# Performance work log

Measured on AMD Instinct MI355X. Metric: run time of the kernel, lower is better.

## Reference

```python
import jax, jax.numpy as jnp
import numpy as np

N = 200000
SIZE = 16384
IN = 128
OUT = 128
HEADS = 4
SLOPE = 0.01  # nn.LeakyReLU default


def setup_inputs() -> dict:
    key = jax.random.key(0)
    ks = jax.random.split(key, 12)
    s = 0.05
    inp = {
        "fea": jax.random.normal(ks[0], (N, IN), jnp.float32),
        "cry_fea": jax.random.normal(ks[1], (SIZE, IN), jnp.float32),
        # MH_M: per-head MLP in->in->out (grouped conv1d k=1, groups=heads)
        "W_m1": jax.random.normal(ks[2], (HEADS, IN, IN), jnp.float32) * s,
        "b_m1": jax.random.normal(ks[3], (HEADS, IN), jnp.float32) * s,
        "W_m2": jax.random.normal(ks[4], (HEADS, OUT, IN), jnp.float32) * s,
        "b_m2": jax.random.normal(ks[5], (HEADS, OUT), jnp.float32) * s,
        # MH_A: per-head MLP 2*in->in->1 (scalar attention, vector_attention=False)
        "W_a1": jax.random.normal(ks[6], (HEADS, IN, 2 * IN), jnp.float32) * s,
        "b_a1": jax.random.normal(ks[7], (HEADS, IN), jnp.float32) * s,
        "W_a2": jax.random.normal(ks[8], (HEADS, 1, IN), jnp.float32) * s,
        "b_a2": jax.random.normal(ks[9], (HEADS, 1), jnp.float32) * s,
        "index": jnp.sort(jax.random.randint(ks[10], (N,), 0, SIZE, jnp.int32)),
        "size": SIZE,
    }
    return inp


def _leaky(x):
    return jnp.where(x >= 0, x, SLOPE * x)


def _mh_mlp(x, W1, b1, W2, b2):
    # x: [N, d_in]; per-head linear -> leaky -> linear. Returns [N, H, d_out].
    h = _leaky(jnp.einsum("ni,hoi->nho", x, W1) + b1)
    return jnp.einsum("nhi,hoi->nho", h, W2) + b2


def reference(fea, cry_fea, W_m1, b_m1, W_m2, b_m2, W_a1, b_a1, W_a2, b_a2, index, size):
    # message transform m: [N, H, OUT]
    m = _mh_mlp(fea, W_m1, b_m1, W_m2, b_m2)
    # attention input: concat(node fea, gathered crystal fea) -> [N, 2*IN]
    a_in = jnp.concatenate([fea, cry_fea[index]], axis=-1)
    alpha = _mh_mlp(a_in, W_a1, b_a1, W_a2, b_a2)  # [N, H, 1]
    # segment (per-crystal) softmax over nodes sharing the same index
    amax = jax.ops.segment_max(alpha, index, num_segments=size)
    amax = jnp.where(jnp.isfinite(amax), amax, 0.0)
    e = jnp.exp(alpha - amax[index])
    denom = jax.ops.segment_sum(e, index, num_segments=size)
    alpha = e / (denom[index] + 1e-16)
    # weighted scatter-add aggregation -> [size, H*OUT]
    out = jax.ops.segment_sum((alpha * m).reshape(-1, HEADS * OUT), index, num_segments=size)
    return out
```

## Files before the change

### kernel.cpp

```cpp
#include <hip/hip_runtime.h>

typedef __bf16 bf16x8 __attribute__((ext_vector_type(8)));
typedef float  f32x4  __attribute__((ext_vector_type(4)));
typedef unsigned int u32x4 __attribute__((ext_vector_type(4)));

#define MFMA(a, b, c) __builtin_amdgcn_mfma_f32_16x16x32_bf16((a), (b), (c), 0, 0, 0)

#define THREADS 512
#define WAVES   8
#define CPW     4
#define CPB     32
#define MT      32

#define SEG_INTS  16416
#define SEG_BYTES (SEG_INTS * 4)
#define O_WM1 0
#define O_WM2 65536
#define O_WA1 131072
#define O_WA2 262144
#define W_ELEMS 262656
#define W_BYTES (W_ELEMS * 2)

#define LA1B 0
#define LM1B 65536
#define LM2B 98304

__device__ __forceinline__ bf16x8 cvt8(const float* pf) {
    float4 a = *(const float4*)pf, b = *(const float4*)(pf + 4);
    bf16x8 o;
    o[0] = (__bf16)a.x; o[1] = (__bf16)a.y; o[2] = (__bf16)a.z; o[3] = (__bf16)a.w;
    o[4] = (__bf16)b.x; o[5] = (__bf16)b.y; o[6] = (__bf16)b.z; o[7] = (__bf16)b.w;
    return o;
}

__device__ __forceinline__ unsigned pk2(float a, float b) {
    unsigned short ua = __builtin_bit_cast(unsigned short, (__bf16)a);
    unsigned short ub = __builtin_bit_cast(unsigned short, (__bf16)b);
    return (unsigned)ua | ((unsigned)ub << 16);
}

__device__ __forceinline__ int lower_bound(const int* __restrict__ a, int n, int v) {
    int lo = 0, hi = n;
    while (lo < hi) { int mid = (lo + hi) >> 1; if (a[mid] < v) lo = mid + 1; else hi = mid; }
    return lo;
}

__global__ __launch_bounds__(256) void prep_kernel(
    const float* __restrict__ Wm1, const float* __restrict__ Wm2,
    const float* __restrict__ Wa1, const float* __restrict__ Wa2,
    __bf16* __restrict__ wb)
{
    int i8 = blockIdx.x * 256 + threadIdx.x;
    if (i8 >= W_ELEMS / 8) return;
    int i = i8 * 8;
    const float* src; int s;
    if      (i < O_WM2) { src = Wm1; s = i; }
    else if (i < O_WA1) { src = Wm2; s = i - O_WM2; }
    else if (i < O_WA2) { src = Wa1; s = i - O_WA1; }
    else                { src = Wa2; s = i - O_WA2; }
    *(bf16x8*)(wb + i) = cvt8(src + s);
}

__global__ __launch_bounds__(256) void seg_kernel(
    const int* __restrict__ index, int N, int S, int* __restrict__ seg)
{
    int c = blockIdx.x * 256 + threadIdx.x;
    if (c <= S) seg[c] = lower_bound(index, N, c);
}

__global__ __launch_bounds__(256) void cast_kernel(
    const float* __restrict__ src, __bf16* __restrict__ dst, int n8)
{
    int i = blockIdx.x * 256 + threadIdx.x;
    if (i < n8) *(bf16x8*)(dst + (size_t)i * 8) = cvt8(src + (size_t)i * 8);
}

template<bool WB, bool SEG, bool FB>
__global__ __launch_bounds__(THREADS, 2) void fused4_kernel(
    const float* __restrict__ fea, const float* __restrict__ cry,
    const float* __restrict__ Wm1, const float* __restrict__ bm1,
    const float* __restrict__ Wm2, const float* __restrict__ bm2,
    const float* __restrict__ Wa1, const float* __restrict__ ba1,
    const float* __restrict__ Wa2, const float* __restrict__ ba2,
    const __bf16* __restrict__ wb, const int* __restrict__ seg,
    const __bf16* __restrict__ feab, const __bf16* __restrict__ cryb,
    const int* __restrict__ index, int N, int S, float* __restrict__ out)
{
    __shared__ __align__(16) __bf16 wlds[65536];
    __shared__ float crylds[WAVES][CPW][128];
    __shared__ float bm1lds[128];

    const int h  = blockIdx.x & 3;
    const int c0 = (blockIdx.x >> 2) * CPB;
    const int t  = threadIdx.x;
    const int lane = t & 63, w = t >> 6, ml = lane & 15, q = lane >> 4;
    const int swzb = (ml & 7) << 4;
    const char* wbytes = (const char*)wlds;

#pragma unroll
    for (int i = 0; i < 16; i++) {
        const int cb = (t + i * THREADS) << 4;
        int local, row, slot, rowE; size_t wboff; const float* basef;
        if (cb < LM1B)      { local = cb;        row = local >> 9; slot = (local >> 4) & 31; rowE = 256; wboff = (size_t)O_WA1 + (size_t)h * 32768; basef = Wa1 + (size_t)h * 32768; }
        else if (cb < LM2B) { local = cb - LM1B; row = local >> 8; slot = (local >> 4) & 15; rowE = 128; wboff = (size_t)O_WM1 + (size_t)h * 16384; basef = Wm1 + (size_t)h * 16384; }
        else                { local = cb - LM2B; row = local >> 8; slot = (local >> 4) & 15; rowE = 128; wboff = (size_t)O_WM2 + (size_t)h * 16384; basef = Wm2 + (size_t)h * 16384; }
        size_t off = (size_t)row * rowE + (size_t)((slot ^ (row & 7)) << 3);
        bf16x8 v;
        if constexpr (WB) v = *(const bf16x8*)(wb + wboff + off);
        else              v = cvt8(basef + off);
        *(bf16x8*)((char*)wlds + cb) = v;
    }
    if (t < 32) *(float4*)&bm1lds[t * 4] = *(const float4*)&bm1[h * 128 + t * 4];
    __syncthreads();

    const int cw0 = min(c0 + w * CPW, S);
    const int cw1 = min(cw0 + CPW, S);
    int start, end;
    if constexpr (SEG) { start = seg[cw0]; end = seg[cw1]; }
    else { start = lower_bound(index, N, cw0); end = lower_bound(index, N, cw1); }

    float ba1v[8], bb2[8], wa2v[8];
#pragma unroll
    for (int ot = 0; ot < 8; ot++) {
        ba1v[ot] = ba1[h * 128 + ot * 16 + ml];
        bb2[ot]  = bm2[h * 128 + ot * 16 + ml];
        wa2v[ot] = Wa2[h * 128 + ot * 16 + ml];
    }
    const float ba2v = ba2[h];

    {
        bf16x8 cf[4];
#pragma unroll
        for (int kk = 0; kk < 4; kk++) {
            bf16x8 z;
#pragma unroll
            for (int j = 0; j < 8; j++) z[j] = (__bf16)0.f;
            if (ml < CPW && cw0 + ml < S) {
                if constexpr (FB) z = *(const bf16x8*)(cryb + (size_t)(cw0 + ml) * 128 + kk * 32 + q * 8);
                else              z = cvt8(cry + (size_t)(cw0 + ml) * 128 + kk * 32 + q * 8);
            }
            cf[kk] = z;
        }
#pragma unroll
        for (int ot = 0; ot < 8; ot++) {
            f32x4 acc = {0.f, 0.f, 0.f, 0.f};
#pragma unroll
            for (int kk = 0; kk < 4; kk++) {
                bf16x8 B = *(const bf16x8*)(wbytes + LA1B + (ot * 16 + ml) * 512 + ((((16 + kk * 4 + q) << 4)) ^ swzb));
                acc = MFMA(cf[kk], B, acc);
            }
            if (q == 0) {
#pragma unroll
                for (int r = 0; r < 4; r++) crylds[w][r][ot * 16 + ml] = acc[r];
            }
        }
    }

    float m_run = -1e30f, d_run = 0.f;
    float wacc[8] = {0.f,0.f,0.f,0.f,0.f,0.f,0.f,0.f};
    int cur_c = -1, emit_c = cw0;

    auto flushf = [&]() {
        float inv = 1.f / (d_run + 1e-16f);
        for (int z = emit_c; z < cur_c; z++)
            *(float2*)&out[(size_t)z * 512 + h * 128 + lane * 2] = make_float2(0.f, 0.f);
#pragma unroll
        for (int ot = 0; ot < 8; ot++) {
            float v = wacc[ot];
            v += __shfl_xor(v, 16);
            v += __shfl_xor(v, 32);
            if (q == 0) out[(size_t)cur_c * 512 + h * 128 + ot * 16 + ml] = v * inv;
            wacc[ot] = 0.f;
        }
        emit_c = cur_c + 1;
        m_run = -1e30f; d_run = 0.f;
    };

    for (int tb = start; tb < end; tb += MT) {
        int nv = end - tb; if (nv > MT) nv = MT;

        const int iv = (lane < nv) ? index[tb + lane] : cw0;

        unsigned long long bmask;
        {
            int ivp = __shfl(iv, lane > 0 ? lane - 1 : 0);
            bmask = __ballot(lane < nv && (lane == 0 || iv != ivp));
        }

        for (int s = 0; s < 2; s++) {
            const int lo = s * 16;
            if (lo >= nv) break;
            int hcnt = nv - lo; if (hcnt > 16) hcnt = 16;

            bf16x8 afh[4];
            {
                const int row = lo + ml;
                const bool val = row < nv;
#pragma unroll
                for (int kk = 0; kk < 4; kk++) {
                    bf16x8 z;
#pragma unroll
                    for (int j = 0; j < 8; j++) z[j] = (__bf16)0.f;
                    if (val) {
                        if constexpr (FB) z = *(const bf16x8*)(feab + (size_t)(tb + row) * 128 + kk * 32 + q * 8);
                        else              z = cvt8(fea + (size_t)(tb + row) * 128 + kk * 32 + q * 8);
                    }
                    afh[kk] = z;
                }
            }

            float lv4[4];
            {
                int cl4[4];
#pragma unroll
                for (int r = 0; r < 4; r++)
                    cl4[r] = __shfl(iv, lo + q * 4 + r) - cw0;
                float lsum[4] = {0.f, 0.f, 0.f, 0.f};
#pragma unroll
                for (int ot = 0; ot < 8; ot++) {
                    bf16x8 B[4];
#pragma unroll
                    for (int kk = 0; kk < 4; kk++)
                        B[kk] = *(const bf16x8*)(wbytes + LA1B + (ot * 16 + ml) * 512 + ((((kk * 4 + q) << 4)) ^ swzb));
                    const int oc = ot * 16 + ml;
                    f32x4 acc;
#pragma unroll
                    for (int r = 0; r < 4; r++) acc[r] = crylds[w][cl4[r]][oc];
#pragma unroll
                    for (int kk = 0; kk < 4; kk++) acc = MFMA(afh[kk], B[kk], acc);
#pragma unroll
                    for (int r = 0; r < 4; r++) {
                        float v = acc[r] + ba1v[ot]; v = v >= 0.f ? v : 0.01f * v;
                        lsum[r] += v * wa2v[ot];
                    }
                }
#pragma unroll
                for (int rr = 0; rr < 4; rr++) {
                    float x = lsum[rr];
                    x += __shfl_xor(x, 1); x += __shfl_xor(x, 2);
                    x += __shfl_xor(x, 4); x += __shfl_xor(x, 8);
                    lv4[rr] = x + ba2v;
                }
            }

            bf16x8 a2h[4];
#pragma unroll
            for (int kk = 0; kk < 4; kk++) {
                unsigned pw[2][2];
#pragma unroll
                for (int otl = 0; otl < 2; otl++) {
                    const int ot = kk * 2 + otl;
                    bf16x8 A[4];
#pragma unroll
                    for (int k4 = 0; k4 < 4; k4++)
                        A[k4] = *(const bf16x8*)(wbytes + LM1B + (ot * 16 + ml) * 256 + ((((k4 * 4 + q) << 4)) ^ swzb));
                    const float4 bq = *(const float4*)&bm1lds[ot * 16 + q * 4];
                    f32x4 acc = {0.f, 0.f, 0.f, 0.f};
#pragma unroll
                    for (int k4 = 0; k4 < 4; k4++) acc = MFMA(A[k4], afh[k4], acc);
                    float v0 = acc[0] + bq.x, v1 = acc[1] + bq.y;
                    float v2 = acc[2] + bq.z, v3 = acc[3] + bq.w;
                    v0 = v0 >= 0.f ? v0 : 0.01f * v0;  v1 = v1 >= 0.f ? v1 : 0.01f * v1;
                    v2 = v2 >= 0.f ? v2 : 0.01f * v2;  v3 = v3 >= 0.f ? v3 : 0.01f * v3;
                    pw[otl][0] = pk2(v0, v1);
                    pw[otl][1] = pk2(v2, v3);
                }
                const int srcLo = (((2 * q) & 3) << 4) + ml;
                const int srcHi = (((2 * q + 1) & 3) << 4) + ml;
                const bool hiSel = (q >> 1) & 1;
                unsigned l0a = (unsigned)__shfl((int)pw[0][0], srcLo);
                unsigned l0b = (unsigned)__shfl((int)pw[1][0], srcLo);
                unsigned l1a = (unsigned)__shfl((int)pw[0][1], srcLo);
                unsigned l1b = (unsigned)__shfl((int)pw[1][1], srcLo);
                unsigned h0a = (unsigned)__shfl((int)pw[0][0], srcHi);
                unsigned h0b = (unsigned)__shfl((int)pw[1][0], srcHi);
                unsigned h1a = (unsigned)__shfl((int)pw[0][1], srcHi);
                unsigned h1b = (unsigned)__shfl((int)pw[1][1], srcHi);
                u32x4 wv4u = { hiSel ? l0b : l0a, hiSel ? l1b : l1a,
                               hiSel ? h0b : h0a, hiSel ? h1b : h1a };
                a2h[kk] = __builtin_bit_cast(bf16x8, wv4u);
            }

            f32x4 acc2h[8];
#pragma unroll
            for (int ot = 0; ot < 8; ot++) {
                bf16x8 B[4];
#pragma unroll
                for (int kk = 0; kk < 4; kk++)
                    B[kk] = *(const bf16x8*)(wbytes + LM2B + (ot * 16 + ml) * 256 + ((((kk * 4 + q) << 4)) ^ swzb));
                f32x4 acc = {bb2[ot], bb2[ot], bb2[ot], bb2[ot]};
#pragma unroll
                for (int kk = 0; kk < 4; kk++) acc = MFMA(a2h[kk], B[kk], acc);
                acc2h[ot] = acc;
            }

            unsigned hm = (unsigned)((bmask >> lo) & 0xffffull) | 1u;
            if (hcnt < 16) hm &= (1u << hcnt) - 1u;
            while (hm) {
                int a = (int)__builtin_ctz(hm);
                hm &= hm - 1u;
                int b = hm ? (int)__builtin_ctz(hm) : hcnt;
                int c = __shfl(iv, lo + a);
                if (c != cur_c) {
                    if (cur_c >= 0) flushf();
                    cur_c = c;
                }
                float tmax = -1e30f;
#pragma unroll
                for (int rr = 0; rr < 4; rr++) {
                    int row = q * 4 + rr;
                    if (row >= a && row < b) tmax = fmaxf(tmax, lv4[rr]);
                }
                tmax = fmaxf(tmax, __shfl_xor(tmax, 16));
                tmax = fmaxf(tmax, __shfl_xor(tmax, 32));
                float m_new = fmaxf(m_run, tmax);
                float scf = __expf(m_run - m_new);
                d_run *= scf;
#pragma unroll
                for (int ot = 0; ot < 8; ot++) wacc[ot] *= scf;
                m_run = m_new;

                float wv4[4]; float dp = 0.f;
#pragma unroll
                for (int rr = 0; rr < 4; rr++) {
                    int row = q * 4 + rr;
                    float ww = (row >= a && row < b) ? __expf(lv4[rr] - m_run) : 0.f;
                    wv4[rr] = ww; dp += ww;
                }
                dp += __shfl_xor(dp, 16);
                dp += __shfl_xor(dp, 32);
                d_run += dp;
#pragma unroll
                for (int ot = 0; ot < 8; ot++) {
                    f32x4 acc = acc2h[ot];
                    wacc[ot] += wv4[0] * acc[0] + wv4[1] * acc[1]
                              + wv4[2] * acc[2] + wv4[3] * acc[3];
                }
            }
        }
    }

    if (cur_c >= 0) flushf();
    for (int z = emit_c; z < cw1; z++)
        *(float2*)&out[(size_t)z * 512 + h * 128 + lane * 2] = make_float2(0.f, 0.f);
}

extern "C" void kernel_launch(void* const* d_in, const int* in_sizes, int n_in,
                              void* d_out, int out_size, void* d_ws, size_t ws_size,
                              hipStream_t stream)
{
    const float* fea = (const float*)d_in[0];
    const float* cry = (const float*)d_in[1];
    const float* Wm1 = (const float*)d_in[2];
    const float* bm1 = (const float*)d_in[3];
    const float* Wm2 = (const float*)d_in[4];
    const float* bm2 = (const float*)d_in[5];
    const float* Wa1 = (const float*)d_in[6];
    const float* ba1 = (const float*)d_in[7];
    const float* Wa2 = (const float*)d_in[8];
    const float* ba2 = (const float*)d_in[9];
    const int* index = (const int*)d_in[10];

    const int N = in_sizes[0] / 128;
    const int S = out_size / 512;
    const int grid = 4 * ((S + CPB - 1) / CPB);

    const size_t wOff    = (size_t)SEG_BYTES;
    const size_t cryOff  = wOff + (size_t)W_BYTES;
    const size_t feaOff  = cryOff + (size_t)S * 256;
    const size_t needSeg  = (size_t)SEG_BYTES;
    const size_t needW    = cryOff;
    const size_t needFull = feaOff + (size_t)N * 256;
    const bool segFits = (S + 1) <= SEG_INTS;

    if (segFits && ws_size >= needFull) {
        int* seg = (int*)d_ws;
        __bf16* wbp  = (__bf16*)((char*)d_ws + wOff);
        __bf16* cryb = (__bf16*)((char*)d_ws + cryOff);
        __bf16* feab = (__bf16*)((char*)d_ws + feaOff);
        seg_kernel<<<(S + 1 + 255) / 256, 256, 0, stream>>>(index, N, S, seg);
        prep_kernel<<<(W_ELEMS / 8 + 255) / 256, 256, 0, stream>>>(Wm1, Wm2, Wa1, Wa2, wbp);
        cast_kernel<<<(S * 16 + 255) / 256, 256, 0, stream>>>(cry, cryb, S * 16);
        cast_kernel<<<(N * 16 + 255) / 256, 256, 0, stream>>>(fea, feab, N * 16);
        fused4_kernel<true, true, true><<<grid, THREADS, 0, stream>>>(
            fea, cry, Wm1, bm1, Wm2, bm2, Wa1, ba1, Wa2, ba2,
            wbp, seg, feab, cryb, index, N, S, (float*)d_out);
    } else if (segFits && ws_size >= needW) {
        int* seg = (int*)d_ws;
        __bf16* wbp = (__bf16*)((char*)d_ws + wOff);
        seg_kernel<<<(S + 1 + 255) / 256, 256, 0, stream>>>(index, N, S, seg);
        prep_kernel<<<(W_ELEMS / 8 + 255) / 256, 256, 0, stream>>>(Wm1, Wm2, Wa1, Wa2, wbp);
        fused4_kernel<true, true, false><<<grid, THREADS, 0, stream>>>(
            fea, cry, Wm1, bm1, Wm2, bm2, Wa1, ba1, Wa2, ba2,
            wbp, seg, nullptr, nullptr, index, N, S, (float*)d_out);
    } else if (segFits && ws_size >= needSeg) {
        int* seg = (int*)d_ws;
        seg_kernel<<<(S + 1 + 255) / 256, 256, 0, stream>>>(index, N, S, seg);
        fused4_kernel<false, true, false><<<grid, THREADS, 0, stream>>>(
            fea, cry, Wm1, bm1, Wm2, bm2, Wa1, ba1, Wa2, ba2,
            nullptr, seg, nullptr, nullptr, index, N, S, (float*)d_out);
    } else {
        fused4_kernel<false, false, false><<<grid, THREADS, 0, stream>>>(
            fea, cry, Wm1, bm1, Wm2, bm2, Wa1, ba1, Wa2, ba2,
            nullptr, nullptr, nullptr, nullptr, index, N, S, (float*)d_out);
    }
}
```

Before: 411.3 us.

## Drop fp32-to-bf16 activation cast kernels, merge prep launches, shrink LDS weights

Removes the separate kernels that cast fea and cry_fea to bf16. The fused kernel now reads fp32 activations and converts them in-register, which avoids a full extra read and write pass over the 200k-row feature matrix. The seg and weight-pack kernels are merged into one launch. Only the node half of Wa1 is now kept in LDS (the crystal half is read from global memory), cutting shared memory to 96KB. That lets blocks grow to 1024 threads and 64 crystals each, with a higher occupancy hint. The cost is twice the global bytes for fea inside the main kernel and uncached global reads for the crystal-side weights.

```diff
diff --git a/kernel.cpp b/kernel.cpp
--- a/kernel.cpp
+++ b/kernel.cpp
@@ -6,10 +6,10 @@
 
 #define MFMA(a, b, c) __builtin_amdgcn_mfma_f32_16x16x32_bf16((a), (b), (c), 0, 0, 0)
 
-#define THREADS 512
-#define WAVES   8
+#define THREADS 1024
+#define WAVES   16
 #define CPW     4
-#define CPB     32
+#define CPB     64
 #define MT      32
 
 #define SEG_INTS  16416
@@ -22,8 +22,8 @@
 #define W_BYTES (W_ELEMS * 2)
 
 #define LA1B 0
-#define LM1B 65536
-#define LM2B 98304
+#define LM1B 32768
+#define LM2B 65536
 
 __device__ __forceinline__ bf16x8 cvt8(const float* pf) {
     float4 a = *(const float4*)pf, b = *(const float4*)(pf + 4);
@@ -45,48 +45,40 @@
     return lo;
 }
 
-__global__ __launch_bounds__(256) void prep_kernel(
+__global__ __launch_bounds__(256) void prep2_kernel(
     const float* __restrict__ Wm1, const float* __restrict__ Wm2,
     const float* __restrict__ Wa1, const float* __restrict__ Wa2,
-    __bf16* __restrict__ wb)
+    const int* __restrict__ index, int N, int S, int segBlocks,
+    int* __restrict__ seg, __bf16* __restrict__ wb, int doPack)
 {
-    int i8 = blockIdx.x * 256 + threadIdx.x;
-    if (i8 >= W_ELEMS / 8) return;
-    int i = i8 * 8;
-    const float* src; int s;
-    if      (i < O_WM2) { src = Wm1; s = i; }
-    else if (i < O_WA1) { src = Wm2; s = i - O_WM2; }
-    else if (i < O_WA2) { src = Wa1; s = i - O_WA1; }
-    else                { src = Wa2; s = i - O_WA2; }
-    *(bf16x8*)(wb + i) = cvt8(src + s);
-}
-
-__global__ __launch_bounds__(256) void seg_kernel(
-    const int* __restrict__ index, int N, int S, int* __restrict__ seg)
-{
-    int c = blockIdx.x * 256 + threadIdx.x;
-    if (c <= S) seg[c] = lower_bound(index, N, c);
-}
-
-__global__ __launch_bounds__(256) void cast_kernel(
-    const float* __restrict__ src, __bf16* __restrict__ dst, int n8)
-{
-    int i = blockIdx.x * 256 + threadIdx.x;
-    if (i < n8) *(bf16x8*)(dst + (size_t)i * 8) = cvt8(src + (size_t)i * 8);
-}
-
-template<bool WB, bool SEG, bool FB>
-__global__ __launch_bounds__(THREADS, 2) void fused4_kernel(
+    const int b = blockIdx.x;
+    if (b < segBlocks) {
+        int c = b * 256 + threadIdx.x;
+        if (c <= S) seg[c] = lower_bound(index, N, c);
+    } else if (doPack) {
+        int i8 = (b - segBlocks) * 256 + threadIdx.x;
+        if (i8 >= W_ELEMS / 8) return;
+        int i = i8 * 8;
+        const float* src; int s;
+        if      (i < O_WM2) { src = Wm1; s = i; }
+        else if (i < O_WA1) { src = Wm2; s = i - O_WM2; }
+        else if (i < O_WA2) { src = Wa1; s = i - O_WA1; }
+        else                { src = Wa2; s = i - O_WA2; }
+        *(bf16x8*)(wb + i) = cvt8(src + s);
+    }
+}
+
+template<bool WB, bool SEG>
+__global__ __launch_bounds__(THREADS, 4) void fused5_kernel(
     const float* __restrict__ fea, const float* __restrict__ cry,
     const float* __restrict__ Wm1, const float* __restrict__ bm1,
     const float* __restrict__ Wm2, const float* __restrict__ bm2,
     const float* __restrict__ Wa1, const float* __restrict__ ba1,
     const float* __restrict__ Wa2, const float* __restrict__ ba2,
     const __bf16* __restrict__ wb, const int* __restrict__ seg,
-    const __bf16* __restrict__ feab, const __bf16* __restrict__ cryb,
     const int* __restrict__ index, int N, int S, float* __restrict__ out)
 {
-    __shared__ __align__(16) __bf16 wlds[65536];
+    __shared__ __align__(16) __bf16 wlds[49152];
     __shared__ float crylds[WAVES][CPW][128];
     __shared__ float bm1lds[128];
 
@@ -98,16 +90,23 @@
     const char* wbytes = (const char*)wlds;
 
 #pragma unroll
-    for (int i = 0; i < 16; i++) {
+    for (int i = 0; i < 6; i++) {
         const int cb = (t + i * THREADS) << 4;
-        int local, row, slot, rowE; size_t wboff; const float* basef;
-        if (cb < LM1B)      { local = cb;        row = local >> 9; slot = (local >> 4) & 31; rowE = 256; wboff = (size_t)O_WA1 + (size_t)h * 32768; basef = Wa1 + (size_t)h * 32768; }
-        else if (cb < LM2B) { local = cb - LM1B; row = local >> 8; slot = (local >> 4) & 15; rowE = 128; wboff = (size_t)O_WM1 + (size_t)h * 16384; basef = Wm1 + (size_t)h * 16384; }
-        else                { local = cb - LM2B; row = local >> 8; slot = (local >> 4) & 15; rowE = 128; wboff = (size_t)O_WM2 + (size_t)h * 16384; basef = Wm2 + (size_t)h * 16384; }
-        size_t off = (size_t)row * rowE + (size_t)((slot ^ (row & 7)) << 3);
+        const int r = cb >> 15;
+        const int local = cb & 32767;
+        const int row = local >> 8;
+        const int col8 = ((((local >> 4) & 15) ^ (row & 7)) << 3);
         bf16x8 v;
-        if constexpr (WB) v = *(const bf16x8*)(wb + wboff + off);
-        else              v = cvt8(basef + off);
+        if (r == 0) {
+            if constexpr (WB) v = *(const bf16x8*)(wb + O_WA1 + (size_t)h * 32768 + row * 256 + col8);
+            else              v = cvt8(Wa1 + (size_t)h * 32768 + (size_t)row * 256 + col8);
+        } else if (r == 1) {
+            if constexpr (WB) v = *(const bf16x8*)(wb + O_WM1 + (size_t)h * 16384 + row * 128 + col8);
+            else              v = cvt8(Wm1 + (size_t)h * 16384 + (size_t)row * 128 + col8);
+        } else {
+            if constexpr (WB) v = *(const bf16x8*)(wb + O_WM2 + (size_t)h * 16384 + row * 128 + col8);
+            else              v = cvt8(Wm2 + (size_t)h * 16384 + (size_t)row * 128 + col8);
+        }
         *(bf16x8*)((char*)wlds + cb) = v;
     }
     if (t < 32) *(float4*)&bm1lds[t * 4] = *(const float4*)&bm1[h * 128 + t * 4];
@@ -135,10 +134,8 @@
             bf16x8 z;
 #pragma unroll
             for (int j = 0; j < 8; j++) z[j] = (__bf16)0.f;
-            if (ml < CPW && cw0 + ml < S) {
-                if constexpr (FB) z = *(const bf16x8*)(cryb + (size_t)(cw0 + ml) * 128 + kk * 32 + q * 8);
-                else              z = cvt8(cry + (size_t)(cw0 + ml) * 128 + kk * 32 + q * 8);
-            }
+            if (ml < CPW && cw0 + ml < S)
+                z = cvt8(cry + (size_t)(cw0 + ml) * 128 + kk * 32 + q * 8);
             cf[kk] = z;
         }
 #pragma unroll
@@ -146,7 +143,10 @@
             f32x4 acc = {0.f, 0.f, 0.f, 0.f};
 #pragma unroll
             for (int kk = 0; kk < 4; kk++) {
-                bf16x8 B = *(const bf16x8*)(wbytes + LA1B + (ot * 16 + ml) * 512 + ((((16 + kk * 4 + q) << 4)) ^ swzb));
+                bf16x8 B;
+                size_t off = (size_t)h * 32768 + (size_t)(ot * 16 + ml) * 256 + 128 + kk * 32 + q * 8;
+                if constexpr (WB) B = *(const bf16x8*)(wb + O_WA1 + off);
+                else              B = cvt8(Wa1 + off);
                 acc = MFMA(cf[kk], B, acc);
             }
             if (q == 0) {
@@ -201,10 +201,7 @@
                     bf16x8 z;
 #pragma unroll
                     for (int j = 0; j < 8; j++) z[j] = (__bf16)0.f;
-                    if (val) {
-                        if constexpr (FB) z = *(const bf16x8*)(feab + (size_t)(tb + row) * 128 + kk * 32 + q * 8);
-                        else              z = cvt8(fea + (size_t)(tb + row) * 128 + kk * 32 + q * 8);
-                    }
+                    if (val) z = cvt8(fea + (size_t)(tb + row) * 128 + kk * 32 + q * 8);
                     afh[kk] = z;
                 }
             }
@@ -221,7 +218,7 @@
                     bf16x8 B[4];
 #pragma unroll
                     for (int kk = 0; kk < 4; kk++)
-                        B[kk] = *(const bf16x8*)(wbytes + LA1B + (ot * 16 + ml) * 512 + ((((kk * 4 + q) << 4)) ^ swzb));
+                        B[kk] = *(const bf16x8*)(wbytes + LA1B + (ot * 16 + ml) * 256 + ((((kk * 4 + q) << 4)) ^ swzb));
                     const int oc = ot * 16 + ml;
                     f32x4 acc;
 #pragma unroll
@@ -365,43 +362,30 @@
     const int S = out_size / 512;
     const int grid = 4 * ((S + CPB - 1) / CPB);
 
-    const size_t wOff    = (size_t)SEG_BYTES;
-    const size_t cryOff  = wOff + (size_t)W_BYTES;
-    const size_t feaOff  = cryOff + (size_t)S * 256;
+    const int segBlocks  = (S + 1 + 255) / 256;
+    const int packBlocks = (W_ELEMS / 8 + 255) / 256;
+    const bool segFits = (S + 1) <= SEG_INTS;
     const size_t needSeg  = (size_t)SEG_BYTES;
-    const size_t needW    = cryOff;
-    const size_t needFull = feaOff + (size_t)N * 256;
-    const bool segFits = (S + 1) <= SEG_INTS;
+    const size_t needFull = (size_t)SEG_BYTES + (size_t)W_BYTES;
 
     if (segFits && ws_size >= needFull) {
         int* seg = (int*)d_ws;
-        __bf16* wbp  = (__bf16*)((char*)d_ws + wOff);
-        __bf16* cryb = (__bf16*)((char*)d_ws + cryOff);
-        __bf16* feab = (__bf16*)((char*)d_ws + feaOff);
-        seg_kernel<<<(S + 1 + 255) / 256, 256, 0, stream>>>(index, N, S, seg);
-        prep_kernel<<<(W_ELEMS / 8 + 255) / 256, 256, 0, stream>>>(Wm1, Wm2, Wa1, Wa2, wbp);
-        cast_kernel<<<(S * 16 + 255) / 256, 256, 0, stream>>>(cry, cryb, S * 16);
-        cast_kernel<<<(N * 16 + 255) / 256, 256, 0, stream>>>(fea, feab, N * 16);
-        fused4_kernel<true, true, true><<<grid, THREADS, 0, stream>>>(
+        __bf16* wbp = (__bf16*)((char*)d_ws + SEG_BYTES);
+        prep2_kernel<<<segBlocks + packBlocks, 256, 0, stream>>>(
+            Wm1, Wm2, Wa1, Wa2, index, N, S, segBlocks, seg, wbp, 1);
+        fused5_kernel<true, true><<<grid, THREADS, 0, stream>>>(
             fea, cry, Wm1, bm1, Wm2, bm2, Wa1, ba1, Wa2, ba2,
-            wbp, seg, feab, cryb, index, N, S, (float*)d_out);
-    } else if (segFits && ws_size >= needW) {
-        int* seg = (int*)d_ws;
-        __bf16* wbp = (__bf16*)((char*)d_ws + wOff);
-        seg_kernel<<<(S + 1 + 255) / 256, 256, 0, stream>>>(index, N, S, seg);
-        prep_kernel<<<(W_ELEMS / 8 + 255) / 256, 256, 0, stream>>>(Wm1, Wm2, Wa1, Wa2, wbp);
-        fused4_kernel<true, true, false><<<grid, THREADS, 0, stream>>>(
-            fea, cry, Wm1, bm1, Wm2, bm2, Wa1, ba1, Wa2, ba2,
-            wbp, seg, nullptr, nullptr, index, N, S, (float*)d_out);
+            wbp, seg, index, N, S, (float*)d_out);
     } else if (segFits && ws_size >= needSeg) {
         int* seg = (int*)d_ws;
-        seg_kernel<<<(S + 1 + 255) / 256, 256, 0, stream>>>(index, N, S, seg);
-        fused4_kernel<false, true, false><<<grid, THREADS, 0, stream>>>(
+        prep2_kernel<<<segBlocks, 256, 0, stream>>>(
+            Wm1, Wm2, Wa1, Wa2, index, N, S, segBlocks, seg, nullptr, 0);
+        fused5_kernel<false, true><<<grid, THREADS, 0, stream>>>(
             fea, cry, Wm1, bm1, Wm2, bm2, Wa1, ba1, Wa2, ba2,
-            nullptr, seg, nullptr, nullptr, index, N, S, (float*)d_out);
+            nullptr, seg, index, N, S, (float*)d_out);
     } else {
-        fused4_kernel<false, false, false><<<grid, THREADS, 0, stream>>>(
+        fused5_kernel<false, false><<<grid, THREADS, 0, stream>>>(
             fea, cry, Wm1, bm1, Wm2, bm2, Wa1, ba1, Wa2, ba2,
-            nullptr, nullptr, nullptr, nullptr, index, N, S, (float*)d_out);
-    }
-}
+            nullptr, nullptr, index, N, S, (float*)d_out);
+    }
+}
```

New measurement: 511.7 us. 24.4% more time.
